# Performance work log

Measured on AMD Instinct MI355X. Metric: run time of the kernel, lower is better.

Reference implementation:

```python
import jax, jax.numpy as jnp
import numpy as np
import math

NUM_HEADS = 16

def _skew(QEr):
    # QEr: [B, H, S, S] -> pad 1 on left of last dim, reshape, drop first row
    B, H, S, _ = QEr.shape
    padded = jnp.pad(QEr, ((0, 0), (0, 0), (0, 0), (1, 0)))  # [B,H,S,S+1]
    reshaped = padded.reshape(B, H, S + 1, S)
    return reshaped[:, :, 1:, :]  # [B,H,S,S]

def setup_inputs() -> dict:
    key = jax.random.key(0)
    ks = jax.random.split(key, 8)
    B, S, D, dh = 4, 1024, 1024, 64
    x = jax.random.normal(ks[0], (B, S, D), dtype=jnp.float32)
    scale = 1.0 / math.sqrt(D)
    Wq = jax.random.normal(ks[1], (D, D), dtype=jnp.float32) * scale
    Wk = jax.random.normal(ks[2], (D, D), dtype=jnp.float32) * scale
    Wv = jax.random.normal(ks[3], (D, D), dtype=jnp.float32) * scale
    bq = jnp.zeros((D,), dtype=jnp.float32)
    bk = jnp.zeros((D,), dtype=jnp.float32)
    bv = jnp.zeros((D,), dtype=jnp.float32)
    Er = jax.random.normal(ks[4], (S, dh), dtype=jnp.float32)
    return {"x": x, "Wq": Wq, "bq": bq, "Wk": Wk, "bk": bk, "Wv": Wv, "bv": bv, "Er": Er}

def reference(x, Wq, bq, Wk, bk, Wv, bv, Er):
    B, S, D = x.shape
    H = NUM_HEADS
    dh = D // H
    # Linear projections (torch Linear: x @ W.T + b)
    q = (x @ Wq.T + bq).reshape(B, S, H, dh).transpose(0, 2, 1, 3)  # [B,H,S,dh]
    k = (x @ Wk.T + bk).reshape(B, S, H, dh).transpose(0, 2, 1, 3)
    v = (x @ Wv.T + bv).reshape(B, S, H, dh).transpose(0, 2, 1, 3)
    # Relative position term: q @ Er^T then skew (start = max_len - S = 0)
    QEr = jnp.einsum('bhsd,td->bhst', q, Er)  # [B,H,S,S]
    Srel = _skew(QEr)
    QKt = jnp.einsum('bhsd,bhtd->bhst', q, k)  # [B,H,S,S]
    attn = (QKt + Srel) / math.sqrt(dh)
    causal = jnp.tril(jnp.ones((S, S), dtype=bool))
    attn = jnp.where(causal[None, None], attn, jnp.float32(-1e6))
    attn = jax.nn.softmax(attn, axis=-1)
    out = jnp.einsum('bhst,bhtd->bhsd', attn, v)  # [B,H,S,dh]
    out = out.transpose(0, 2, 1, 3).reshape(B, S, D)
    return out  # dropout is identity in eval / p=0
```

## Files before the change

kernel.cpp:

```cpp
#include <hip/hip_runtime.h>
#include <stdint.h>

#define S_LEN 1024
#define DM 1024
#define NH 16
#define DH 64
#define NB 4

typedef unsigned short u16;
typedef __attribute__((ext_vector_type(8))) short short8;
typedef __attribute__((ext_vector_type(4))) float f32x4;
typedef __attribute__((ext_vector_type(4))) unsigned int u32x4;

__device__ __forceinline__ u16 f2bf(float f) {
  union { float f; unsigned int u; } c;
  c.f = f;
  unsigned int u = c.u;
  return (u16)((u + 0x7fffu + ((u >> 16) & 1u)) >> 16);
}

__device__ __forceinline__ void g2l16(const void* g, void* l) {
  __builtin_amdgcn_global_load_lds(
      (const __attribute__((address_space(1))) unsigned int*)(uintptr_t)g,
      (__attribute__((address_space(3))) unsigned int*)(uint32_t)(uintptr_t)l,
      16, 0, 0);
}

__global__ __launch_bounds__(256) void cvt_f32_bf16(
    const float* __restrict__ x, const float* __restrict__ Wq,
    const float* __restrict__ Wk, const float* __restrict__ Wv,
    const float* __restrict__ Er, u16* __restrict__ xb,
    u16* __restrict__ Wqb, u16* __restrict__ Wkb, u16* __restrict__ Wvb,
    u16* __restrict__ Erb) {
  const size_t f = ((size_t)blockIdx.x * 256 + threadIdx.x) * 8;
  const float* src;
  u16* dst;
  size_t off;
  if (f < 4194304) { src = x; dst = xb; off = f; }
  else if (f < 5242880) { src = Wq; dst = Wqb; off = f - 4194304; }
  else if (f < 6291456) { src = Wk; dst = Wkb; off = f - 5242880; }
  else if (f < 7340032) { src = Wv; dst = Wvb; off = f - 6291456; }
  else { src = Er; dst = Erb; off = f - 7340032; }
  const float4 a = *(const float4*)(src + off);
  const float4 b = *(const float4*)(src + off + 4);
  u16 o[8] = {f2bf(a.x), f2bf(a.y), f2bf(a.z), f2bf(a.w),
              f2bf(b.x), f2bf(b.y), f2bf(b.z), f2bf(b.w)};
  *(u32x4*)(dst + off) = *(const u32x4*)o;
}

__global__ __launch_bounds__(256) void qkv_gemm(
    const u16* __restrict__ x,
    const u16* __restrict__ Wq, const float* __restrict__ bq,
    const u16* __restrict__ Wk, const float* __restrict__ bk,
    const u16* __restrict__ Wv, const float* __restrict__ bv,
    u16* __restrict__ Qo, u16* __restrict__ Ko, u16* __restrict__ Vo) {
  __shared__ __attribute__((aligned(16))) u16 Al[128 * 32];
  __shared__ __attribute__((aligned(16))) u16 Bl[128 * 32];

  const int tid = threadIdx.x;
  const int lane = tid & 63;
  const int wave = tid >> 6;
  const int z = blockIdx.z;
  const u16* W = (z == 0) ? Wq : (z == 1) ? Wk : Wv;
  const float* bias = (z == 0) ? bq : (z == 1) ? bk : bv;

  const int m0 = blockIdx.y * 128;
  const int n0 = blockIdx.x * 128;

  f32x4 acc[4][4];
  const f32x4 fzero = {0.f, 0.f, 0.f, 0.f};
#pragma unroll
  for (int i = 0; i < 4; i++)
#pragma unroll
    for (int j = 0; j < 4; j++) acc[i][j] = fzero;

  const int srow = tid >> 2;
  const int schunk = tid & 3;
  const u16* gA = x + (size_t)(m0 + srow) * DM + schunk * 8;
  const u16* gB = W + (size_t)(n0 + srow) * DM + schunk * 8;

  const int fr = lane & 15;
  const int fq = lane >> 4;
  const int wr = (wave >> 1) * 64;
  const int wc = (wave & 1) * 64;

  for (int k = 0; k < DM; k += 32) {
    g2l16(gA + k, &Al[tid * 8]);
    g2l16(gA + (size_t)64 * DM + k, &Al[2048 + tid * 8]);
    g2l16(gB + k, &Bl[tid * 8]);
    g2l16(gB + (size_t)64 * DM + k, &Bl[2048 + tid * 8]);
    __syncthreads();
    short8 a[4], b[4];
#pragma unroll
    for (int i = 0; i < 4; i++)
      a[i] = *(const short8*)&Al[(wr + i * 16 + fr) * 32 + fq * 8];
#pragma unroll
    for (int j = 0; j < 4; j++)
      b[j] = *(const short8*)&Bl[(wc + j * 16 + fr) * 32 + fq * 8];
#pragma unroll
    for (int i = 0; i < 4; i++)
#pragma unroll
      for (int j = 0; j < 4; j++)
        acc[i][j] =
            __builtin_amdgcn_mfma_f32_16x16x32_bf16(a[i], b[j], acc[i][j], 0, 0, 0);
    __syncthreads();
  }

#pragma unroll
  for (int j = 0; j < 4; j++) {
    const int n = n0 + wc + j * 16 + fr;
    const float bsv = bias[n];
    const int h = n >> 6, d = n & (DH - 1);
#pragma unroll
    for (int i = 0; i < 4; i++) {
#pragma unroll
      for (int r = 0; r < 4; r++) {
        const int m = m0 + wr + i * 16 + fq * 4 + r;
        const int bb = m >> 10, s = m & (S_LEN - 1);
        const u16 o = f2bf(acc[i][j][r] + bsv);
        if (z == 2)
          Vo[((size_t)(bb * NH + h) * DH + d) * S_LEN + s] = o;
        else if (z == 1)
          Ko[((size_t)(bb * NH + h) * S_LEN + s) * DH + d] = o;
        else
          Qo[((size_t)(bb * NH + h) * S_LEN + s) * DH + d] = o;
      }
    }
  }
}

__global__ __launch_bounds__(512, 4) void attn(
    const u16* __restrict__ Q, const u16* __restrict__ K,
    const u16* __restrict__ Vt, const u16* __restrict__ Er,
    float* __restrict__ out) {
  __shared__ __attribute__((aligned(16))) u16 El[192 * 72];
  __shared__ __attribute__((aligned(16))) u16 Kl[64 * 72];
  __shared__ __attribute__((aligned(16))) u16 Vl[64 * 72];
  __shared__ __attribute__((aligned(16))) u16 Pl[8 * 16 * 72];

  const int tid = threadIdx.x;
  const int lane = tid & 63;
  const int w = tid >> 6;
  const int bh = blockIdx.y;
  const int b = bh >> 4, h = bh & (NH - 1);
  const int it = (blockIdx.y < 32) ? (int)blockIdx.x : 7 - (int)blockIdx.x;
  const int i0 = it * 128;

  const u16* Qb = Q + (size_t)bh * S_LEN * DH;
  const u16* Kb = K + (size_t)bh * S_LEN * DH;
  const u16* Vb = Vt + (size_t)bh * DH * S_LEN;
  u16* Pw = Pl + w * 16 * 72;

  const int sr = tid >> 3;
  const int sc = (tid & 7) * 8;

  *(u32x4*)&El[sr * 72 + sc] = *(const u32x4*)&Qb[(i0 + sr) * DH + sc];
  *(u32x4*)&El[(sr + 64) * 72 + sc] =
      *(const u32x4*)&Qb[(i0 + sr + 64) * DH + sc];
  __syncthreads();

  const int fr = lane & 15;
  const int fq = lane >> 4;
  short8 aq0 = *(const short8*)&El[(w * 16 + fr) * 72 + fq * 8];
  short8 aq1 = *(const short8*)&El[(w * 16 + fr) * 72 + 32 + fq * 8];
  __syncthreads();

  float mrow[4], lrow[4];
  f32x4 accO[4];
  const f32x4 fzero = {0.f, 0.f, 0.f, 0.f};
#pragma unroll
  for (int r = 0; r < 4; r++) { mrow[r] = -3.0e38f; lrow[r] = 0.f; }
#pragma unroll
  for (int t = 0; t < 4; t++) accO[t] = fzero;

  for (int j0 = 0; j0 <= i0 + 64; j0 += 64) {
    *(u32x4*)&Kl[sr * 72 + sc] = *(const u32x4*)&Kb[(j0 + sr) * DH + sc];
    *(u32x4*)&Vl[sr * 72 + sc] = *(const u32x4*)&Vb[sr * S_LEN + j0 + sc];
    const int E0 = S_LEN - 128 - i0 + j0;
#pragma unroll
    for (int qq = 0; qq < 3; qq++) {
      const int g = sr + 64 * qq;
      int e = E0 + g;
      e = (e > S_LEN - 1) ? (S_LEN - 1) : e;
      *(u32x4*)&El[g * 72 + sc] = *(const u32x4*)&Er[e * DH + sc];
    }
    __syncthreads();

    if (j0 <= i0 + w * 16 + 15) {
      f32x4 sfr[4];
#pragma unroll
      for (int t = 0; t < 4; t++) {
        short8 b0 = *(const short8*)&Kl[(t * 16 + fr) * 72 + fq * 8];
        short8 b1 = *(const short8*)&Kl[(t * 16 + fr) * 72 + 32 + fq * 8];
        f32x4 zz = fzero;
        zz = __builtin_amdgcn_mfma_f32_16x16x32_bf16(aq0, b0, zz, 0, 0, 0);
        zz = __builtin_amdgcn_mfma_f32_16x16x32_bf16(aq1, b1, zz, 0, 0, 0);
        sfr[t] = zz;
      }

      f32x4 zz[5];
#pragma unroll
      for (int f = 0; f < 5; f++) {
        const int er = 112 - w * 16 + f * 16 + fr;
        short8 b0 = *(const short8*)&El[er * 72 + fq * 8];
        short8 b1 = *(const short8*)&El[er * 72 + 32 + fq * 8];
        f32x4 t0 = fzero;
        t0 = __builtin_amdgcn_mfma_f32_16x16x32_bf16(aq0, b0, t0, 0, 0, 0);
        t0 = __builtin_amdgcn_mfma_f32_16x16x32_bf16(aq1, b1, t0, 0, 0, 0);
        zz[f] = t0;
      }

      float p[4][4];
#pragma unroll
      for (int r = 0; r < 4; r++) {
        const int row = fq * 4 + r;
        const int c = 15 - row + fr;
        const int src = (fq << 4) | (c & 15);
        float sh[5];
#pragma unroll
        for (int f = 0; f < 5; f++) sh[f] = __shfl(zz[f][r], src);
#pragma unroll
        for (int t = 0; t < 4; t++) {
          const float rel = (c < 16) ? sh[t] : sh[t + 1];
          float sv = (sfr[t][r] + rel) * 0.125f;
          const int jj = j0 + t * 16 + fr;
          const int ii = i0 + w * 16 + row;
          if (jj > ii) sv = -3.0e38f;
          p[t][r] = sv;
        }
      }

#pragma unroll
      for (int r = 0; r < 4; r++) {
        float rm = fmaxf(fmaxf(p[0][r], p[1][r]), fmaxf(p[2][r], p[3][r]));
#pragma unroll
        for (int off = 1; off < 16; off <<= 1)
          rm = fmaxf(rm, __shfl_xor(rm, off));
        const float mnew = fmaxf(mrow[r], rm);
        const float alpha = __expf(mrow[r] - mnew);
        mrow[r] = mnew;
        float rs = 0.f;
#pragma unroll
        for (int t = 0; t < 4; t++) {
          const float e = __expf(p[t][r] - mnew);
          p[t][r] = e;
          rs += e;
        }
#pragma unroll
        for (int off = 1; off < 16; off <<= 1) rs += __shfl_xor(rs, off);
        lrow[r] = lrow[r] * alpha + rs;
#pragma unroll
        for (int t = 0; t < 4; t++) accO[t][r] *= alpha;
      }

#pragma unroll
      for (int t = 0; t < 4; t++)
#pragma unroll
        for (int r = 0; r < 4; r++)
          Pw[(fq * 4 + r) * 72 + t * 16 + fr] = f2bf(p[t][r]);
      __builtin_amdgcn_s_waitcnt(0xC07F);

      short8 ap0 = *(const short8*)&Pw[fr * 72 + fq * 8];
      short8 ap1 = *(const short8*)&Pw[fr * 72 + 32 + fq * 8];
#pragma unroll
      for (int t = 0; t < 4; t++) {
        short8 b0 = *(const short8*)&Vl[(t * 16 + fr) * 72 + fq * 8];
        short8 b1 = *(const short8*)&Vl[(t * 16 + fr) * 72 + 32 + fq * 8];
        accO[t] =
            __builtin_amdgcn_mfma_f32_16x16x32_bf16(ap0, b0, accO[t], 0, 0, 0);
        accO[t] =
            __builtin_amdgcn_mfma_f32_16x16x32_bf16(ap1, b1, accO[t], 0, 0, 0);
      }
    }
    __syncthreads();
  }

#pragma unroll
  for (int r = 0; r < 4; r++) {
    const float inv = 1.f / lrow[r];
    const int s = i0 + w * 16 + fq * 4 + r;
#pragma unroll
    for (int t = 0; t < 4; t++) {
      const int d = t * 16 + fr;
      out[((size_t)b * S_LEN + s) * DM + h * DH + d] = accO[t][r] * inv;
    }
  }
}

extern "C" void kernel_launch(void* const* d_in, const int* in_sizes, int n_in,
                              void* d_out, int out_size, void* d_ws, size_t ws_size,
                              hipStream_t stream) {
  const float* x = (const float*)d_in[0];
  const float* Wq = (const float*)d_in[1];
  const float* bq = (const float*)d_in[2];
  const float* Wk = (const float*)d_in[3];
  const float* bk = (const float*)d_in[4];
  const float* Wv = (const float*)d_in[5];
  const float* bv = (const float*)d_in[6];
  const float* Er = (const float*)d_in[7];
  float* out = (float*)d_out;

  const size_t per = (size_t)NB * NH * S_LEN * DH;
  u16* Qw = (u16*)d_ws;
  u16* Kw = Qw + per;
  u16* Vw = Kw + per;
  u16* xb = Vw + per;
  u16* Wqb = xb + per;
  u16* Wkb = Wqb + (size_t)DM * DM;
  u16* Wvb = Wkb + (size_t)DM * DM;
  u16* Erb = Wvb + (size_t)DM * DM;

  cvt_f32_bf16<<<3616, 256, 0, stream>>>(x, Wq, Wk, Wv, Er, xb, Wqb, Wkb, Wvb,
                                         Erb);
  dim3 g1(DM / 128, (NB * S_LEN) / 128, 3);
  qkv_gemm<<<g1, dim3(256), 0, stream>>>(xb, Wqb, bq, Wkb, bk, Wvb, bv, Qw, Kw,
                                         Vw);
  dim3 g2(8, NB * NH);
  attn<<<g2, dim3(512), 0, stream>>>(Qw, Kw, Vw, Erb, out);
}
```

Before: 182.6 us.

## Load K, V and Er fragments directly from global memory, dropping shared staging

The attention kernel stops staging K, V and the Er window through shared memory with block-wide barriers. Each wave now loads its MFMA operands directly from global memory (relying on caches), runs its own causal loop length, and reuses the last Er fragment across iterations. Blocks shrink to 256 threads over 64 query rows, the grid doubles, and the P scratch uses an XOR swizzle to avoid bank conflicts. This removes __syncthreads and idle waves past the diagonal, at the cost of redundant global/L2 traffic with uncoalesced per-lane 16-byte loads.

```diff
diff --git a/kernel.cpp b/kernel.cpp
--- a/kernel.cpp
+++ b/kernel.cpp
@@ -129,41 +129,43 @@
   }
 }
 
-__global__ __launch_bounds__(512, 4) void attn(
+__device__ __forceinline__ f32x4 er_frag(const u16* __restrict__ Er, int e0,
+                                         int fr, int fq, short8 aq0,
+                                         short8 aq1) {
+  int e = e0 + fr;
+  e = (e > S_LEN - 1) ? (S_LEN - 1) : e;
+  const short8 b0 = *(const short8*)&Er[(size_t)e * DH + fq * 8];
+  const short8 b1 = *(const short8*)&Er[(size_t)e * DH + 32 + fq * 8];
+  f32x4 z = {0.f, 0.f, 0.f, 0.f};
+  z = __builtin_amdgcn_mfma_f32_16x16x32_bf16(aq0, b0, z, 0, 0, 0);
+  z = __builtin_amdgcn_mfma_f32_16x16x32_bf16(aq1, b1, z, 0, 0, 0);
+  return z;
+}
+
+__global__ __launch_bounds__(256, 3) void attn(
     const u16* __restrict__ Q, const u16* __restrict__ K,
     const u16* __restrict__ Vt, const u16* __restrict__ Er,
     float* __restrict__ out) {
-  __shared__ __attribute__((aligned(16))) u16 El[192 * 72];
-  __shared__ __attribute__((aligned(16))) u16 Kl[64 * 72];
-  __shared__ __attribute__((aligned(16))) u16 Vl[64 * 72];
-  __shared__ __attribute__((aligned(16))) u16 Pl[8 * 16 * 72];
+  __shared__ __attribute__((aligned(16))) u16 Pl[4][16 * 72];
 
   const int tid = threadIdx.x;
   const int lane = tid & 63;
   const int w = tid >> 6;
   const int bh = blockIdx.y;
   const int b = bh >> 4, h = bh & (NH - 1);
-  const int it = (blockIdx.y < 32) ? (int)blockIdx.x : 7 - (int)blockIdx.x;
-  const int i0 = it * 128;
+  const int rt = (bh < 32) ? (int)blockIdx.x : 15 - (int)blockIdx.x;
+  const int i0 = rt * 64 + w * 16;
 
   const u16* Qb = Q + (size_t)bh * S_LEN * DH;
   const u16* Kb = K + (size_t)bh * S_LEN * DH;
   const u16* Vb = Vt + (size_t)bh * DH * S_LEN;
-  u16* Pw = Pl + w * 16 * 72;
-
-  const int sr = tid >> 3;
-  const int sc = (tid & 7) * 8;
-
-  *(u32x4*)&El[sr * 72 + sc] = *(const u32x4*)&Qb[(i0 + sr) * DH + sc];
-  *(u32x4*)&El[(sr + 64) * 72 + sc] =
-      *(const u32x4*)&Qb[(i0 + sr + 64) * DH + sc];
-  __syncthreads();
+  u16* Pw = Pl[w];
 
   const int fr = lane & 15;
   const int fq = lane >> 4;
-  short8 aq0 = *(const short8*)&El[(w * 16 + fr) * 72 + fq * 8];
-  short8 aq1 = *(const short8*)&El[(w * 16 + fr) * 72 + 32 + fq * 8];
-  __syncthreads();
+
+  const short8 aq0 = *(const short8*)&Qb[(size_t)(i0 + fr) * DH + fq * 8];
+  const short8 aq1 = *(const short8*)&Qb[(size_t)(i0 + fr) * DH + 32 + fq * 8];
 
   float mrow[4], lrow[4];
   f32x4 accO[4];
@@ -173,112 +175,105 @@
 #pragma unroll
   for (int t = 0; t < 4; t++) accO[t] = fzero;
 
-  for (int j0 = 0; j0 <= i0 + 64; j0 += 64) {
-    *(u32x4*)&Kl[sr * 72 + sc] = *(const u32x4*)&Kb[(j0 + sr) * DH + sc];
-    *(u32x4*)&Vl[sr * 72 + sc] = *(const u32x4*)&Vb[sr * S_LEN + j0 + sc];
-    const int E0 = S_LEN - 128 - i0 + j0;
-#pragma unroll
-    for (int qq = 0; qq < 3; qq++) {
-      const int g = sr + 64 * qq;
-      int e = E0 + g;
-      e = (e > S_LEN - 1) ? (S_LEN - 1) : e;
-      *(u32x4*)&El[g * 72 + sc] = *(const u32x4*)&Er[e * DH + sc];
-    }
-    __syncthreads();
-
-    if (j0 <= i0 + w * 16 + 15) {
-      f32x4 sfr[4];
+  f32x4 zzc = fzero;
+
+  for (int j0 = 0; j0 <= i0 + 15; j0 += 64) {
+    const int eb = S_LEN - 16 - i0 + j0;
+
+    f32x4 sfr[4];
+#pragma unroll
+    for (int t = 0; t < 4; t++) {
+      const short8 b0 =
+          *(const short8*)&Kb[(size_t)(j0 + t * 16 + fr) * DH + fq * 8];
+      const short8 b1 =
+          *(const short8*)&Kb[(size_t)(j0 + t * 16 + fr) * DH + 32 + fq * 8];
+      f32x4 z = fzero;
+      z = __builtin_amdgcn_mfma_f32_16x16x32_bf16(aq0, b0, z, 0, 0, 0);
+      z = __builtin_amdgcn_mfma_f32_16x16x32_bf16(aq1, b1, z, 0, 0, 0);
+      sfr[t] = z;
+    }
+
+    f32x4 zz[5];
+    if (j0 == 0)
+      zz[0] = er_frag(Er, eb, fr, fq, aq0, aq1);
+    else
+      zz[0] = zzc;
+#pragma unroll
+    for (int f = 1; f < 5; f++)
+      zz[f] = er_frag(Er, eb + f * 16, fr, fq, aq0, aq1);
+    zzc = zz[4];
+
+    float p[4][4];
+#pragma unroll
+    for (int r = 0; r < 4; r++) {
+      const int row = fq * 4 + r;
+      const int c = 15 - row + fr;
+      const int src = (fq << 4) | (c & 15);
+      float sh[5];
+#pragma unroll
+      for (int f = 0; f < 5; f++) sh[f] = __shfl(zz[f][r], src);
 #pragma unroll
       for (int t = 0; t < 4; t++) {
-        short8 b0 = *(const short8*)&Kl[(t * 16 + fr) * 72 + fq * 8];
-        short8 b1 = *(const short8*)&Kl[(t * 16 + fr) * 72 + 32 + fq * 8];
-        f32x4 zz = fzero;
-        zz = __builtin_amdgcn_mfma_f32_16x16x32_bf16(aq0, b0, zz, 0, 0, 0);
-        zz = __builtin_amdgcn_mfma_f32_16x16x32_bf16(aq1, b1, zz, 0, 0, 0);
-        sfr[t] = zz;
+        const float rel = (c < 16) ? sh[t] : sh[t + 1];
+        float sv = (sfr[t][r] + rel) * 0.125f;
+        const int jj = j0 + t * 16 + fr;
+        const int ii = i0 + row;
+        if (jj > ii) sv = -3.0e38f;
+        p[t][r] = sv;
       }
-
-      f32x4 zz[5];
-#pragma unroll
-      for (int f = 0; f < 5; f++) {
-        const int er = 112 - w * 16 + f * 16 + fr;
-        short8 b0 = *(const short8*)&El[er * 72 + fq * 8];
-        short8 b1 = *(const short8*)&El[er * 72 + 32 + fq * 8];
-        f32x4 t0 = fzero;
-        t0 = __builtin_amdgcn_mfma_f32_16x16x32_bf16(aq0, b0, t0, 0, 0, 0);
-        t0 = __builtin_amdgcn_mfma_f32_16x16x32_bf16(aq1, b1, t0, 0, 0, 0);
-        zz[f] = t0;
+    }
+
+#pragma unroll
+    for (int r = 0; r < 4; r++) {
+      float rm = fmaxf(fmaxf(p[0][r], p[1][r]), fmaxf(p[2][r], p[3][r]));
+#pragma unroll
+      for (int off = 1; off < 16; off <<= 1)
+        rm = fmaxf(rm, __shfl_xor(rm, off));
+      const float mnew = fmaxf(mrow[r], rm);
+      const float alpha = __expf(mrow[r] - mnew);
+      mrow[r] = mnew;
+      float rs = 0.f;
+#pragma unroll
+      for (int t = 0; t < 4; t++) {
+        const float e = __expf(p[t][r] - mnew);
+        p[t][r] = e;
+        rs += e;
       }
-
-      float p[4][4];
-#pragma unroll
-      for (int r = 0; r < 4; r++) {
-        const int row = fq * 4 + r;
-        const int c = 15 - row + fr;
-        const int src = (fq << 4) | (c & 15);
-        float sh[5];
-#pragma unroll
-        for (int f = 0; f < 5; f++) sh[f] = __shfl(zz[f][r], src);
-#pragma unroll
-        for (int t = 0; t < 4; t++) {
-          const float rel = (c < 16) ? sh[t] : sh[t + 1];
-          float sv = (sfr[t][r] + rel) * 0.125f;
-          const int jj = j0 + t * 16 + fr;
-          const int ii = i0 + w * 16 + row;
-          if (jj > ii) sv = -3.0e38f;
-          p[t][r] = sv;
-        }
-      }
-
-#pragma unroll
-      for (int r = 0; r < 4; r++) {
-        float rm = fmaxf(fmaxf(p[0][r], p[1][r]), fmaxf(p[2][r], p[3][r]));
-#pragma unroll
-        for (int off = 1; off < 16; off <<= 1)
-          rm = fmaxf(rm, __shfl_xor(rm, off));
-        const float mnew = fmaxf(mrow[r], rm);
-        const float alpha = __expf(mrow[r] - mnew);
-        mrow[r] = mnew;
-        float rs = 0.f;
-#pragma unroll
-        for (int t = 0; t < 4; t++) {
-          const float e = __expf(p[t][r] - mnew);
-          p[t][r] = e;
-          rs += e;
-        }
-#pragma unroll
-        for (int off = 1; off < 16; off <<= 1) rs += __shfl_xor(rs, off);
-        lrow[r] = lrow[r] * alpha + rs;
-#pragma unroll
-        for (int t = 0; t < 4; t++) accO[t][r] *= alpha;
-      }
-
-#pragma unroll
-      for (int t = 0; t < 4; t++)
-#pragma unroll
-        for (int r = 0; r < 4; r++)
-          Pw[(fq * 4 + r) * 72 + t * 16 + fr] = f2bf(p[t][r]);
-      __builtin_amdgcn_s_waitcnt(0xC07F);
-
-      short8 ap0 = *(const short8*)&Pw[fr * 72 + fq * 8];
-      short8 ap1 = *(const short8*)&Pw[fr * 72 + 32 + fq * 8];
-#pragma unroll
-      for (int t = 0; t < 4; t++) {
-        short8 b0 = *(const short8*)&Vl[(t * 16 + fr) * 72 + fq * 8];
-        short8 b1 = *(const short8*)&Vl[(t * 16 + fr) * 72 + 32 + fq * 8];
-        accO[t] =
-            __builtin_amdgcn_mfma_f32_16x16x32_bf16(ap0, b0, accO[t], 0, 0, 0);
-        accO[t] =
-            __builtin_amdgcn_mfma_f32_16x16x32_bf16(ap1, b1, accO[t], 0, 0, 0);
-      }
-    }
-    __syncthreads();
+#pragma unroll
+      for (int off = 1; off < 16; off <<= 1) rs += __shfl_xor(rs, off);
+      lrow[r] = lrow[r] * alpha + rs;
+#pragma unroll
+      for (int t = 0; t < 4; t++) accO[t][r] *= alpha;
+    }
+
+#pragma unroll
+    for (int t = 0; t < 4; t++)
+#pragma unroll
+      for (int r = 0; r < 4; r++)
+        Pw[(fq * 4 + r) * 72 + ((t ^ fq) * 16 + fr)] = f2bf(p[t][r]);
+    __builtin_amdgcn_s_waitcnt(0xC07F);
+
+    const int rsw = (fr >> 2) << 4;
+    const short8 ap0 = *(const short8*)&Pw[fr * 72 + ((fq * 8) ^ rsw)];
+    const short8 ap1 = *(const short8*)&Pw[fr * 72 + ((32 + fq * 8) ^ rsw)];
+
+#pragma unroll
+    for (int t = 0; t < 4; t++) {
+      const short8 b0 =
+          *(const short8*)&Vb[(size_t)(t * 16 + fr) * S_LEN + j0 + fq * 8];
+      const short8 b1 =
+          *(const short8*)&Vb[(size_t)(t * 16 + fr) * S_LEN + j0 + 32 + fq * 8];
+      accO[t] =
+          __builtin_amdgcn_mfma_f32_16x16x32_bf16(ap0, b0, accO[t], 0, 0, 0);
+      accO[t] =
+          __builtin_amdgcn_mfma_f32_16x16x32_bf16(ap1, b1, accO[t], 0, 0, 0);
+    }
   }
 
 #pragma unroll
   for (int r = 0; r < 4; r++) {
     const float inv = 1.f / lrow[r];
-    const int s = i0 + w * 16 + fq * 4 + r;
+    const int s = i0 + fq * 4 + r;
 #pragma unroll
     for (int t = 0; t < 4; t++) {
       const int d = t * 16 + fr;
@@ -315,6 +310,6 @@
   dim3 g1(DM / 128, (NB * S_LEN) / 128, 3);
   qkv_gemm<<<g1, dim3(256), 0, stream>>>(xb, Wqb, bq, Wkb, bk, Wvb, bv, Qw, Kw,
                                          Vw);
-  dim3 g2(8, NB * NH);
-  attn<<<g2, dim3(512), 0, stream>>>(Qw, Kw, Vw, Erb, out);
-}
+  dim3 g2(16, NB * NH);
+  attn<<<g2, dim3(256), 0, stream>>>(Qw, Kw, Vw, Erb, out);
+}
```

New measurement: 224.0 us. 22.6% more time.

## Use ring buffer for Er tiles and reuse relative-position MFMA results across iterations

Applied to the files above, without the earlier changes.

Er rows are kept in a 192-row circular LDS buffer, so each key-block iteration loads only 64 new rows instead of reloading all 192. The last relative-position MFMA tile from the previous iteration is carried over, which saves one of the five QEr tile products per iteration. Q fragments are now loaded straight from global memory instead of being staged through LDS with two barriers. The P tile store and load now use an XOR swizzle to cut LDS bank conflicts. The carried tile depends on every wave doing the same iterations, and waves that skip their masked tail would leave zzc stale, which adds correctness risk.

```diff
diff --git a/kernel.cpp b/kernel.cpp
--- a/kernel.cpp
+++ b/kernel.cpp
@@ -17,6 +17,10 @@
   c.f = f;
   unsigned int u = c.u;
   return (u16)((u + 0x7fffu + ((u >> 16) & 1u)) >> 16);
+}
+
+__device__ __forceinline__ int m192(int e) {
+  return e - ((e * 21846) >> 22) * 192;
 }
 
 __device__ __forceinline__ void g2l16(const void* g, void* l) {
@@ -143,7 +147,7 @@
   const int w = tid >> 6;
   const int bh = blockIdx.y;
   const int b = bh >> 4, h = bh & (NH - 1);
-  const int it = (blockIdx.y < 32) ? (int)blockIdx.x : 7 - (int)blockIdx.x;
+  const int it = (bh < 32) ? (int)blockIdx.x : 7 - (int)blockIdx.x;
   const int i0 = it * 128;
 
   const u16* Qb = Q + (size_t)bh * S_LEN * DH;
@@ -154,16 +158,13 @@
   const int sr = tid >> 3;
   const int sc = (tid & 7) * 8;
 
-  *(u32x4*)&El[sr * 72 + sc] = *(const u32x4*)&Qb[(i0 + sr) * DH + sc];
-  *(u32x4*)&El[(sr + 64) * 72 + sc] =
-      *(const u32x4*)&Qb[(i0 + sr + 64) * DH + sc];
-  __syncthreads();
-
   const int fr = lane & 15;
   const int fq = lane >> 4;
-  short8 aq0 = *(const short8*)&El[(w * 16 + fr) * 72 + fq * 8];
-  short8 aq1 = *(const short8*)&El[(w * 16 + fr) * 72 + 32 + fq * 8];
-  __syncthreads();
+
+  const short8 aq0 =
+      *(const short8*)&Qb[(size_t)(i0 + w * 16 + fr) * DH + fq * 8];
+  const short8 aq1 =
+      *(const short8*)&Qb[(size_t)(i0 + w * 16 + fr) * DH + 32 + fq * 8];
 
   float mrow[4], lrow[4];
   f32x4 accO[4];
@@ -173,16 +174,27 @@
 #pragma unroll
   for (int t = 0; t < 4; t++) accO[t] = fzero;
 
+  f32x4 zzc = fzero;
+
   for (int j0 = 0; j0 <= i0 + 64; j0 += 64) {
-    *(u32x4*)&Kl[sr * 72 + sc] = *(const u32x4*)&Kb[(j0 + sr) * DH + sc];
-    *(u32x4*)&Vl[sr * 72 + sc] = *(const u32x4*)&Vb[sr * S_LEN + j0 + sc];
     const int E0 = S_LEN - 128 - i0 + j0;
-#pragma unroll
-    for (int qq = 0; qq < 3; qq++) {
-      const int g = sr + 64 * qq;
-      int e = E0 + g;
-      e = (e > S_LEN - 1) ? (S_LEN - 1) : e;
-      *(u32x4*)&El[g * 72 + sc] = *(const u32x4*)&Er[e * DH + sc];
+
+    *(u32x4*)&Kl[sr * 72 + sc] = *(const u32x4*)&Kb[(size_t)(j0 + sr) * DH + sc];
+    *(u32x4*)&Vl[sr * 72 + sc] =
+        *(const u32x4*)&Vb[(size_t)sr * S_LEN + j0 + sc];
+    if (j0 == 0) {
+#pragma unroll
+      for (int qq = 0; qq < 3; qq++) {
+        const int e = E0 + sr + 64 * qq;
+        const int slot = m192(e);
+        const int ec = (e > S_LEN - 1) ? (S_LEN - 1) : e;
+        *(u32x4*)&El[slot * 72 + sc] = *(const u32x4*)&Er[(size_t)ec * DH + sc];
+      }
+    } else {
+      const int e = E0 + 128 + sr;
+      const int slot = m192(e);
+      const int ec = (e > S_LEN - 1) ? (S_LEN - 1) : e;
+      *(u32x4*)&El[slot * 72 + sc] = *(const u32x4*)&Er[(size_t)ec * DH + sc];
     }
     __syncthreads();
 
@@ -192,23 +204,29 @@
       for (int t = 0; t < 4; t++) {
         short8 b0 = *(const short8*)&Kl[(t * 16 + fr) * 72 + fq * 8];
         short8 b1 = *(const short8*)&Kl[(t * 16 + fr) * 72 + 32 + fq * 8];
-        f32x4 zz = fzero;
-        zz = __builtin_amdgcn_mfma_f32_16x16x32_bf16(aq0, b0, zz, 0, 0, 0);
-        zz = __builtin_amdgcn_mfma_f32_16x16x32_bf16(aq1, b1, zz, 0, 0, 0);
-        sfr[t] = zz;
-      }
-
+        f32x4 zv = fzero;
+        zv = __builtin_amdgcn_mfma_f32_16x16x32_bf16(aq0, b0, zv, 0, 0, 0);
+        zv = __builtin_amdgcn_mfma_f32_16x16x32_bf16(aq1, b1, zv, 0, 0, 0);
+        sfr[t] = zv;
+      }
+
+      const int ebm = m192(E0 + 112 - w * 16);
       f32x4 zz[5];
+      const int f0 = (j0 == 0) ? 0 : 1;
 #pragma unroll
       for (int f = 0; f < 5; f++) {
-        const int er = 112 - w * 16 + f * 16 + fr;
-        short8 b0 = *(const short8*)&El[er * 72 + fq * 8];
-        short8 b1 = *(const short8*)&El[er * 72 + 32 + fq * 8];
+        if (f < f0) continue;
+        int row = ebm + f * 16 + fr;
+        row = (row >= 192) ? row - 192 : row;
+        short8 b0 = *(const short8*)&El[row * 72 + fq * 8];
+        short8 b1 = *(const short8*)&El[row * 72 + 32 + fq * 8];
         f32x4 t0 = fzero;
         t0 = __builtin_amdgcn_mfma_f32_16x16x32_bf16(aq0, b0, t0, 0, 0, 0);
         t0 = __builtin_amdgcn_mfma_f32_16x16x32_bf16(aq1, b1, t0, 0, 0, 0);
         zz[f] = t0;
       }
+      if (j0 > 0) zz[0] = zzc;
+      zzc = zz[4];
 
       float p[4][4];
 #pragma unroll
@@ -257,11 +275,13 @@
       for (int t = 0; t < 4; t++)
 #pragma unroll
         for (int r = 0; r < 4; r++)
-          Pw[(fq * 4 + r) * 72 + t * 16 + fr] = f2bf(p[t][r]);
+          Pw[(fq * 4 + r) * 72 + ((t ^ fq) * 16 + fr)] = f2bf(p[t][r]);
       __builtin_amdgcn_s_waitcnt(0xC07F);
 
-      short8 ap0 = *(const short8*)&Pw[fr * 72 + fq * 8];
-      short8 ap1 = *(const short8*)&Pw[fr * 72 + 32 + fq * 8];
+      const int rsw = (fr >> 2) << 4;
+      const short8 ap0 = *(const short8*)&Pw[fr * 72 + ((fq * 8) ^ rsw)];
+      const short8 ap1 = *(const short8*)&Pw[fr * 72 + ((32 + fq * 8) ^ rsw)];
+
 #pragma unroll
       for (int t = 0; t < 4; t++) {
         short8 b0 = *(const short8*)&Vl[(t * 16 + fr) * 72 + fq * 8];
```

After: 174.1 us. -4.7%, faster.
